# Kernel optimization log

Hardware: AMD Instinct MI355X
Metric: run time of the kernel (lower is better)

Reference implementation:

```python
import jax, jax.numpy as jnp
import numpy as np

D = 256      # d_size
Z = 32       # z_size
IN = 256     # input_size
B = 128      # minibatch_size
T = 1000     # seq_len
TAU = 2.0
W = 0.001    # w (KL weight, t>0)
W1 = 0.001   # w1 (KL weight, t==0)
WD1 = 0.001  # wd1 (init-h NLL weight)
EPS = 1e-6


def setup_inputs() -> dict:
    key = jax.random.key(0)
    ks = jax.random.split(key, 11)
    sD = 1.0 / np.sqrt(D)
    sZ = 1.0 / np.sqrt(Z)
    sI = 1.0 / np.sqrt(IN)
    return {
        "hd": jax.random.normal(ks[0], (B, T, IN), jnp.float32),
        "A": jax.random.normal(ks[1], (B, T, 2 * Z), jnp.float32) * 0.1,
        "in_p0": jax.random.normal(ks[2], (B, 2 * Z), jnp.float32) * 0.1,
        "noise": jax.random.normal(ks[3], (B, T, Z), jnp.float32),
        "Wd2h": jax.random.normal(ks[4], (D, D), jnp.float32) * sD,
        "Wz2h": jax.random.normal(ks[5], (D, Z), jnp.float32) * sZ,
        "Wd2z": jax.random.normal(ks[6], (2 * Z, D), jnp.float32) * sD,
        "Whd2h": jax.random.normal(ks[7], (D, IN), jnp.float32) * sI,
        "bias_d": jax.random.normal(ks[8], (D,), jnp.float32) * 0.1,
        "init_h": jax.random.normal(ks[9], (B, D), jnp.float32) * 0.1,
        "init_h_mu": jax.random.normal(ks[10], (D,), jnp.float32) * 0.1,
    }


def reference(hd, A, in_p0, noise, Wd2h, Wz2h, Wd2z, Whd2h, bias_d, init_h, init_h_mu):
    dtype = hd.dtype
    # tau vector: tau everywhere, 2*tau for first half of units
    tau = jnp.full((D,), TAU, dtype=dtype).at[: D // 2].set(2.0 * TAU)
    decay = 1.0 - 1.0 / tau
    inv_tau = 1.0 / tau

    # initialize(): wd1 != 0 -> h = init_h, d = tanh(h)
    h0 = init_h
    d0 = jnp.tanh(h0)

    def step(carry, xs):
        h, d = carry
        t, hd_t, A_t, n_t = xs
        # prior: t==0 uses external in_p, else d_to_z(d)
        dz = d @ Wd2z.T                              # [B, 2Z]
        prior_in = jnp.where(t == 0, in_p0, dz)
        mu_p = jnp.tanh(prior_in[:, :Z])
        sigma_p = jnp.exp(prior_in[:, Z:])
        # posterior from adaptive variables A
        mu_q = jnp.tanh(A_t[:, :Z])
        sigma_q = jnp.exp(A_t[:, Z:])
        # reparameterized sample
        z = mu_q + n_t * sigma_q
        # leaky-integrator MTRNN update
        pre = d @ Wd2h.T + z @ Wz2h.T + hd_t @ Whd2h.T + bias_d
        h_new = decay * h + pre * inv_tau
        d_new = jnp.tanh(h_new)
        # KL(q || p), normalized by z_size
        kl = jnp.sum(
            jnp.log(sigma_p + EPS) - jnp.log(sigma_q + EPS) - 0.5
            + 0.5 * (mu_q**2 + sigma_q**2 - 2.0 * mu_q * mu_p + mu_p**2)
            / (sigma_p**2 + EPS)
        ) / Z
        wkl = jnp.where(t == 0, W1, W) * kl
        return (h_new, d_new), (d_new, wkl)

    ts = jnp.arange(T)
    (_, _), (d_seq, wkls) = jax.lax.scan(
        step,
        (h0, d0),
        (ts, hd.transpose(1, 0, 2), A.transpose(1, 0, 2), noise.transpose(1, 0, 2)),
    )

    # compute_nll_init_h (init_var = 1.0)
    nll_init_h = jnp.sum(
        0.5 * jnp.log(2.0 * jnp.pi) + 0.5 * (init_h - init_h_mu) ** 2
    ) / D
    wnll_init_h = WD1 * nll_init_h

    return d_seq.transpose(1, 0, 2), jnp.sum(wkls), wnll_init_h
```

## Files before the change

kernel.cpp:

```cpp
#include <hip/hip_runtime.h>


#define BB 128
#define TT 1000
#define NSEQ 32768000
#define KEPS 1e-6f

typedef _Float16 half2v __attribute__((ext_vector_type(2)));

__device__ __forceinline__ float bfu(unsigned short u) {
    union { unsigned int i; float f; } v; v.i = ((unsigned int)u) << 16; return v.f;
}
__device__ __forceinline__ unsigned short f2bf(float f) {
    union { float f; unsigned int i; } v; v.f = f;
    unsigned int x = v.i;
    return (unsigned short)((x + 0x7fffu + ((x >> 16) & 1u)) >> 16);
}
__device__ __forceinline__ float ldf(const void* p, size_t i, int bf) {
    return bf ? bfu(((const unsigned short*)p)[i]) : ((const float*)p)[i];
}
__device__ __forceinline__ void stf(void* p, size_t i, float v, int bf) {
    if (bf) ((unsigned short*)p)[i] = f2bf(v);
    else    ((float*)p)[i] = v;
}
__device__ __forceinline__ half2v u2h2(unsigned int u) {
    union { unsigned int u; half2v h; } v; v.u = u; return v.h;
}
__device__ __forceinline__ half2v bfpair2h2(unsigned int u) {
    union { unsigned int i; float f; } lo, hi;
    lo.i = u << 16; hi.i = u & 0xffff0000u;
    half2v r; r.x = (_Float16)lo.f; r.y = (_Float16)hi.f; return r;
}
__device__ __forceinline__ unsigned short f2h_bits(float f) {
    union { _Float16 h; unsigned short u; } v; v.h = (_Float16)f; return v.u;
}

#if __has_builtin(__builtin_amdgcn_fdot2)
#define FDOT2(a, b, c) __builtin_amdgcn_fdot2((a), (b), (c), false)
#else
__device__ __forceinline__ float FDOT2(half2v a, half2v b, float c) {
    return c + (float)a.x * (float)b.x + (float)a.y * (float)b.y;
}
#endif

#define BAR() do {                                             \
    asm volatile("s_waitcnt lgkmcnt(0)" ::: "memory");         \
    __builtin_amdgcn_s_barrier();                              \
    asm volatile("" ::: "memory");                             \
} while (0)

__global__ __launch_bounds__(256) void k0_detect(
    const unsigned short* __restrict__ hd, int* __restrict__ flag)
{
    __shared__ int cnt;
    if (threadIdx.x == 0) cnt = 0;
    __syncthreads();
    int c = 0;
    for (int i = threadIdx.x; i < 2048; i += 256) {
        unsigned short u = hd[i];
        int e = (u >> 7) & 0xFF;
        c += ((e >= 112 && e <= 134) || ((u & 0x7FFF) == 0)) ? 1 : 0;
    }
    atomicAdd(&cnt, c);
    __syncthreads();
    if (threadIdx.x == 0) flag[0] = (cnt > 1700) ? 1 : 0;
}

__global__ __launch_bounds__(256) void k1_gemm(
    const void* __restrict__ hd,
    const void* __restrict__ W,
    const void* __restrict__ bias,
    void* __restrict__ out,
    const int* __restrict__ flagp)
{
    const int bf = flagp[0];
    __shared__ __align__(16) float hdS[32][36];
    const int tid = threadIdx.x;
    const int j = tid;
    const long m0 = (long)blockIdx.x * 32;
    const int lm = tid >> 3;
    const int lk = (tid & 7) * 4;

    float acc[32];
#pragma unroll
    for (int m = 0; m < 32; m++) acc[m] = 0.f;

    for (int kc = 0; kc < 256; kc += 32) {
        float stage[4];
        float w[32];
        if (bf) {
            const unsigned short* hp =
                (const unsigned short*)hd + (size_t)(m0 + lm) * 256 + kc + lk;
            uint2 sv = *(const uint2*)hp;
            stage[0] = bfu((unsigned short)(sv.x & 0xffff));
            stage[1] = bfu((unsigned short)(sv.x >> 16));
            stage[2] = bfu((unsigned short)(sv.y & 0xffff));
            stage[3] = bfu((unsigned short)(sv.y >> 16));
            const unsigned short* wp =
                (const unsigned short*)W + (size_t)j * 256 + kc;
#pragma unroll
            for (int g = 0; g < 4; g++) {
                uint4 wv = *(const uint4*)(wp + g * 8);
                w[g*8+0] = bfu((unsigned short)(wv.x & 0xffff));
                w[g*8+1] = bfu((unsigned short)(wv.x >> 16));
                w[g*8+2] = bfu((unsigned short)(wv.y & 0xffff));
                w[g*8+3] = bfu((unsigned short)(wv.y >> 16));
                w[g*8+4] = bfu((unsigned short)(wv.z & 0xffff));
                w[g*8+5] = bfu((unsigned short)(wv.z >> 16));
                w[g*8+6] = bfu((unsigned short)(wv.w & 0xffff));
                w[g*8+7] = bfu((unsigned short)(wv.w >> 16));
            }
        } else {
            const float* hp = (const float*)hd + (size_t)(m0 + lm) * 256 + kc + lk;
            float4 sv = *(const float4*)hp;
            stage[0] = sv.x; stage[1] = sv.y; stage[2] = sv.z; stage[3] = sv.w;
            const float* wp = (const float*)W + (size_t)j * 256 + kc;
#pragma unroll
            for (int g = 0; g < 8; g++) {
                float4 wv = *(const float4*)(wp + g * 4);
                w[g*4+0] = wv.x; w[g*4+1] = wv.y; w[g*4+2] = wv.z; w[g*4+3] = wv.w;
            }
        }
        __syncthreads();
#pragma unroll
        for (int q = 0; q < 4; q++) hdS[lm][lk + q] = stage[q];
        __syncthreads();
#pragma unroll
        for (int m = 0; m < 32; m++) {
            float s0 = 0.f, s1 = 0.f;
#pragma unroll
            for (int k4 = 0; k4 < 8; k4++) {
                float4 a = *(const float4*)&hdS[m][k4 * 4];
                float t0 = a.x*w[k4*4+0] + a.y*w[k4*4+1];
                float t1 = a.z*w[k4*4+2] + a.w*w[k4*4+3];
                if (k4 & 1) s1 += t0 + t1; else s0 += t0 + t1;
            }
            acc[m] += s0 + s1;
        }
    }
    float bj = ldf(bias, (size_t)j, bf);
#pragma unroll
    for (int m = 0; m < 32; m++)
        stf(out, (size_t)(m0 + m) * 256 + j, acc[m] + bj, bf);
}

__global__ __launch_bounds__(256) void k2_scan_bf(
    const unsigned short* __restrict__ A,
    const unsigned short* __restrict__ noise,
    const unsigned short* __restrict__ Wd2h,
    const unsigned short* __restrict__ Wz2h,
    const unsigned short* __restrict__ init_h,
    unsigned short* __restrict__ out,
    const int* __restrict__ flagp)
{
    if (flagp[0] != 1) return;
    const int b = blockIdx.x;
    const int tid = threadIdx.x;
    const int j = tid;
    const int l = tid & 63;
    const int w = tid >> 6;

    __shared__ unsigned int dPk[2][128];
    __shared__ unsigned int zPk[2][16];

    half2v wdh[128];
    {
        const uint4* wr = (const uint4*)(Wd2h + (size_t)j * 256);
#pragma unroll
        for (int k = 0; k < 32; k++) {
            uint4 q = wr[k];
            wdh[k*4+0] = bfpair2h2(q.x);
            wdh[k*4+1] = bfpair2h2(q.y);
            wdh[k*4+2] = bfpair2h2(q.z);
            wdh[k*4+3] = bfpair2h2(q.w);
        }
    }
    half2v wzh[16];
    {
        const uint4* wr = (const uint4*)(Wz2h + (size_t)j * 32);
#pragma unroll
        for (int k = 0; k < 4; k++) {
            uint4 q = wr[k];
            wzh[k*4+0] = bfpair2h2(q.x);
            wzh[k*4+1] = bfpair2h2(q.y);
            wzh[k*4+2] = bfpair2h2(q.z);
            wzh[k*4+3] = bfpair2h2(q.w);
        }
    }

    float hv = bfu(init_h[(size_t)b * 256 + j]);
    float h = hv;
    const float tau = (j < 128) ? 4.f : 2.f;
    const float decay = 1.f - 1.f / tau;
    const float invt = 1.f / tau;
    {
        float d0 = tanhf(hv);
        unsigned short u16 = f2h_bits(d0);
        int p16 = __shfl_xor((int)u16, 1, 64);
        if (!(tid & 1))
            dPk[0][tid >> 1] =
                (unsigned int)u16 | (((unsigned int)(unsigned short)p16) << 16);
    }

    const size_t baseA = (size_t)b * TT * 64;
    const size_t baseN = (size_t)b * TT * 32;
    const size_t baseO = (size_t)b * TT * 256;

    float aVc = 0.f, nVc = 0.f;
    if (w == 1) {
        float av0 = bfu(A[baseA + l]);
        float val0 = (l < 32) ? tanhf(av0) : expf(av0);
        float nv0 = (l < 32) ? bfu(noise[baseN + l]) : 0.f;
        float e0 = __shfl_down(val0, 32, 64);
        if (l < 32) {
            float z0 = val0 + nv0 * e0;
            unsigned short uz = f2h_bits(z0);
            int pz = __shfl_xor((int)uz, 1, 64);
            if (!(l & 1))
                zPk[0][l >> 1] =
                    (unsigned int)uz | (((unsigned int)(unsigned short)pz) << 16);
        }
        aVc = bfu(A[baseA + 64 + l]);
        nVc = (l < 32) ? bfu(noise[baseN + 32 + l]) : 0.f;
    }

    float hdw_c = bfu(out[baseO + j]);
    BAR();

#pragma unroll 1
    for (int t = 0; t < TT; t++) {
        float hdw_p = 0.f;
        if (t < TT - 1) hdw_p = bfu(out[baseO + (size_t)(t + 1) * 256 + j]);
        float aVp = 0.f, nVp = 0.f;
        if (w == 1 && t + 2 < TT) {
            aVp = bfu(A[baseA + (size_t)(t + 2) * 64 + l]);
            nVp = (l < 32) ? bfu(noise[baseN + (size_t)(t + 2) * 32 + l]) : 0.f;
        }

        float ac[8];
#pragma unroll
        for (int i = 0; i < 8; i++) ac[i] = 0.f;
        {
            const uint4* dp = (const uint4*)dPk[t & 1];
#pragma unroll
            for (int k = 0; k < 32; k++) {
                uint4 q = dp[k];
                const int base = (k & 1) << 2;
                ac[base+0] = FDOT2(u2h2(q.x), wdh[k*4+0], ac[base+0]);
                ac[base+1] = FDOT2(u2h2(q.y), wdh[k*4+1], ac[base+1]);
                ac[base+2] = FDOT2(u2h2(q.z), wdh[k*4+2], ac[base+2]);
                ac[base+3] = FDOT2(u2h2(q.w), wdh[k*4+3], ac[base+3]);
            }
            const uint4* zp = (const uint4*)zPk[t & 1];
#pragma unroll
            for (int k = 0; k < 4; k++) {
                uint4 q = zp[k];
                const int base = (k & 1) << 2;
                ac[base+0] = FDOT2(u2h2(q.x), wzh[k*4+0], ac[base+0]);
                ac[base+1] = FDOT2(u2h2(q.y), wzh[k*4+1], ac[base+1]);
                ac[base+2] = FDOT2(u2h2(q.z), wzh[k*4+2], ac[base+2]);
                ac[base+3] = FDOT2(u2h2(q.w), wzh[k*4+3], ac[base+3]);
            }
        }
        float P = ((ac[0] + ac[1]) + (ac[2] + ac[3]))
                + ((ac[4] + ac[5]) + (ac[6] + ac[7]));

        float pre = P + hdw_c;
        h = decay * h + pre * invt;
        float dn = tanhf(h);
        out[baseO + (size_t)t * 256 + j] = f2bf(dn);
        {
            unsigned short u16 = f2h_bits(dn);
            int p16 = __shfl_xor((int)u16, 1, 64);
            if (!(tid & 1))
                dPk[(t + 1) & 1][tid >> 1] =
                    (unsigned int)u16 | (((unsigned int)(unsigned short)p16) << 16);
        }
        if (w == 1 && t < TT - 1) {
            float val = (l < 32) ? tanhf(aVc) : expf(aVc);
            float e = __shfl_down(val, 32, 64);
            if (l < 32) {
                float zz = val + nVc * e;
                unsigned short uz = f2h_bits(zz);
                int pz = __shfl_xor((int)uz, 1, 64);
                if (!(l & 1))
                    zPk[(t + 1) & 1][l >> 1] =
                        (unsigned int)uz | (((unsigned int)(unsigned short)pz) << 16);
            }
            aVc = aVp; nVc = nVp;
        }
        hdw_c = hdw_p;
        BAR();
    }
}

__global__ __launch_bounds__(512) void k2_scan_f32(
    const float* __restrict__ A,
    const float* __restrict__ noise,
    const float* __restrict__ Wd2h,
    const float* __restrict__ Wz2h,
    const float* __restrict__ init_h,
    float* __restrict__ out,
    const int* __restrict__ flagp)
{
    if (flagp[0] != 0) return;
    const int b = blockIdx.x;
    const int tid = threadIdx.x;
    const int j = tid & 255;
    const int half = tid >> 8;
    const int isz = (tid >= 256 && tid < 288);
    const int zi = tid & 31;

    __shared__ __align__(16) float dS[256];
    __shared__ __align__(16) float zS[2][32];
    __shared__ float pp[2][256];

    float wdh[128];
#pragma unroll
    for (int u = 0; u < 128; u++)
        wdh[u] = Wd2h[(size_t)j * 256 + half * 128 + u];
    float wzh[16];
#pragma unroll
    for (int u = 0; u < 16; u++)
        wzh[u] = Wz2h[(size_t)j * 32 + half * 16 + u];

    const size_t baseA = (size_t)b * TT * 64;
    const size_t baseN = (size_t)b * TT * 32;
    const size_t baseO = (size_t)b * TT * 256;

    float h = 0.f, decay = 0.f, invt = 0.f;
    if (half == 0) {
        float hv = init_h[(size_t)b * 256 + j];
        h = hv;
        float tau = (j < 128) ? 4.f : 2.f;
        decay = 1.f - 1.f / tau;
        invt = 1.f / tau;
        dS[j] = tanhf(hv);
    }

    float aL = 0.f, aH = 0.f, nZ = 0.f;
    if (isz) {
        float a0 = A[baseA + zi];
        float a1 = A[baseA + 32 + zi];
        float n0 = noise[baseN + zi];
        zS[0][zi] = tanhf(a0) + n0 * expf(a1);
        aL = A[baseA + 64 + zi];
        aH = A[baseA + 64 + 32 + zi];
        nZ = noise[baseN + 32 + zi];
    }

    float hdw_c = 0.f;
    if (half == 0) hdw_c = out[baseO + j];
    BAR();

#pragma unroll 1
    for (int t = 0; t < TT; t++) {
        float hdw_p = 0.f;
        if (t < TT - 1 && half == 0)
            hdw_p = out[baseO + (size_t)(t + 1) * 256 + j];
        float aL2 = 0.f, aH2 = 0.f, nZ2 = 0.f;
        if (isz && t + 2 <= TT - 1) {
            aL2 = A[baseA + (size_t)(t + 2) * 64 + zi];
            aH2 = A[baseA + (size_t)(t + 2) * 64 + 32 + zi];
            nZ2 = noise[baseN + (size_t)(t + 2) * 32 + zi];
        }

        float pa0 = 0.f, pa1 = 0.f, pa2 = 0.f, pa3 = 0.f;
        const float* db = dS + half * 128;
#pragma unroll
        for (int g = 0; g < 16; g++) {
            float4 x = *(const float4*)(db + g * 8);
            float4 y = *(const float4*)(db + g * 8 + 4);
            float t0 = x.x*wdh[g*8+0] + x.y*wdh[g*8+1];
            float t1 = x.z*wdh[g*8+2] + x.w*wdh[g*8+3];
            float t2 = y.x*wdh[g*8+4] + y.y*wdh[g*8+5];
            float t3 = y.z*wdh[g*8+6] + y.w*wdh[g*8+7];
            float gs = (t0 + t1) + (t2 + t3);
            if      ((g & 3) == 0) pa0 += gs;
            else if ((g & 3) == 1) pa1 += gs;
            else if ((g & 3) == 2) pa2 += gs;
            else                   pa3 += gs;
        }
        {
            const float* zb = &zS[t & 1][half * 16];
            float4 z0 = *(const float4*)(zb);
            float4 z1 = *(const float4*)(zb + 4);
            float4 z2 = *(const float4*)(zb + 8);
            float4 z3 = *(const float4*)(zb + 12);
            float c0 = z0.x*wzh[0]  + z0.y*wzh[1];
            float c1 = z0.z*wzh[2]  + z0.w*wzh[3];
            float c2 = z1.x*wzh[4]  + z1.y*wzh[5];
            float c3 = z1.z*wzh[6]  + z1.w*wzh[7];
            float c4 = z2.x*wzh[8]  + z2.y*wzh[9];
            float c5 = z2.z*wzh[10] + z2.w*wzh[11];
            float c6 = z3.x*wzh[12] + z3.y*wzh[13];
            float c7 = z3.z*wzh[14] + z3.w*wzh[15];
            pa0 += (c0 + c1) + (c2 + c3);
            pa1 += (c4 + c5) + (c6 + c7);
        }
        pp[half][j] = (pa0 + pa1) + (pa2 + pa3);
        BAR();

        if (half == 0) {
            float pre = pp[0][j] + pp[1][j] + hdw_c;
            h = decay * h + pre * invt;
            float dn = tanhf(h);
            dS[j] = dn;
            out[baseO + (size_t)t * 256 + j] = dn;
        }
        if (isz && t < TT - 1) {
            zS[(t + 1) & 1][zi] = tanhf(aL) + nZ * expf(aH);
            aL = aL2; aH = aH2; nZ = nZ2;
        }
        hdw_c = hdw_p;
        BAR();
    }
}

__global__ __launch_bounds__(256) void k2b_kl(
    const void* __restrict__ dseq,
    const void* __restrict__ A,
    const void* __restrict__ in_p0,
    const void* __restrict__ Wd2z,
    float* __restrict__ ws_kl,
    const int* __restrict__ flagp)
{
    const int bf = flagp[0];
    const int tid = threadIdx.x;
    const long m0 = (long)blockIdx.x * 32;

    __shared__ __align__(16) float hdS[32][36];
    __shared__ float dzS[32][64];
    __shared__ float red[256];

    const int j  = tid & 63;
    const int rg = tid >> 6;

    const int lm = tid >> 3;
    const int lk = (tid & 7) * 4;
    const long gr_lm = m0 + lm;
    const int  t_lm  = (int)(gr_lm % 1000);
    const long prow  = (t_lm == 0) ? gr_lm : gr_lm - 1;

    float acc[8];
#pragma unroll
    for (int m = 0; m < 8; m++) acc[m] = 0.f;

    for (int kc = 0; kc < 256; kc += 32) {
        float stage[4];
        float w[32];
        if (bf) {
            const unsigned short* hp =
                (const unsigned short*)dseq + (size_t)prow * 256 + kc + lk;
            uint2 sv = *(const uint2*)hp;
            stage[0] = bfu((unsigned short)(sv.x & 0xffff));
            stage[1] = bfu((unsigned short)(sv.x >> 16));
            stage[2] = bfu((unsigned short)(sv.y & 0xffff));
            stage[3] = bfu((unsigned short)(sv.y >> 16));
            const unsigned short* wp =
                (const unsigned short*)Wd2z + (size_t)j * 256 + kc;
#pragma unroll
            for (int g = 0; g < 4; g++) {
                uint4 wv = *(const uint4*)(wp + g * 8);
                w[g*8+0] = bfu((unsigned short)(wv.x & 0xffff));
                w[g*8+1] = bfu((unsigned short)(wv.x >> 16));
                w[g*8+2] = bfu((unsigned short)(wv.y & 0xffff));
                w[g*8+3] = bfu((unsigned short)(wv.y >> 16));
                w[g*8+4] = bfu((unsigned short)(wv.z & 0xffff));
                w[g*8+5] = bfu((unsigned short)(wv.z >> 16));
                w[g*8+6] = bfu((unsigned short)(wv.w & 0xffff));
                w[g*8+7] = bfu((unsigned short)(wv.w >> 16));
            }
        } else {
            const float* hp = (const float*)dseq + (size_t)prow * 256 + kc + lk;
            float4 sv = *(const float4*)hp;
            stage[0] = sv.x; stage[1] = sv.y; stage[2] = sv.z; stage[3] = sv.w;
            const float* wp = (const float*)Wd2z + (size_t)j * 256 + kc;
#pragma unroll
            for (int g = 0; g < 8; g++) {
                float4 wv = *(const float4*)(wp + g * 4);
                w[g*4+0] = wv.x; w[g*4+1] = wv.y; w[g*4+2] = wv.z; w[g*4+3] = wv.w;
            }
        }
        __syncthreads();
#pragma unroll
        for (int q = 0; q < 4; q++) hdS[lm][lk + q] = stage[q];
        __syncthreads();
#pragma unroll
        for (int m = 0; m < 8; m++) {
            const int row = rg * 8 + m;
            float s0 = 0.f, s1 = 0.f;
#pragma unroll
            for (int k4 = 0; k4 < 8; k4++) {
                float4 a = *(const float4*)&hdS[row][k4 * 4];
                float t0 = a.x*w[k4*4+0] + a.y*w[k4*4+1];
                float t1 = a.z*w[k4*4+2] + a.w*w[k4*4+3];
                if (k4 & 1) s1 += t0 + t1; else s0 += t0 + t1;
            }
            acc[m] += s0 + s1;
        }
    }
    __syncthreads();
#pragma unroll
    for (int m = 0; m < 8; m++) dzS[rg * 8 + m][j] = acc[m];
    __syncthreads();

    const int zz = tid & 31;
    const int rr = tid >> 5;
    float s = 0.f;
#pragma unroll
    for (int mm = 0; mm < 4; mm++) {
        const int m = rr * 4 + mm;
        const long gr = m0 + m;
        const int  t  = (int)(gr % 1000);
        const long bb = gr / 1000;
        float pin_mu, pin_sg;
        if (t == 0) {
            pin_mu = ldf(in_p0, (size_t)bb * 64 + zz, bf);
            pin_sg = ldf(in_p0, (size_t)bb * 64 + 32 + zz, bf);
        } else {
            pin_mu = dzS[m][zz];
            pin_sg = dzS[m][zz + 32];
        }
        float mp = tanhf(pin_mu);
        float sp = expf(pin_sg);
        float amu = ldf(A, (size_t)gr * 64 + zz, bf);
        float asg = ldf(A, (size_t)gr * 64 + 32 + zz, bf);
        float mq = tanhf(amu);
        float sq = expf(asg);
        s += logf(sp + KEPS) - logf(sq + KEPS) - 0.5f
           + 0.5f * (mq*mq + sq*sq - 2.f*mq*mp + mp*mp) / (sp*sp + KEPS);
    }
    red[tid] = s;
    __syncthreads();
    for (int off = 128; off > 0; off >>= 1) {
        if (tid < off) red[tid] += red[tid + off];
        __syncthreads();
    }
    if (tid == 0) atomicAdd(ws_kl, red[0]);
}

__global__ __launch_bounds__(256) void k3_final(
    const void* __restrict__ init_h,
    const void* __restrict__ init_mu,
    const float* __restrict__ ws_kl,
    void* __restrict__ out,
    const int* __restrict__ flagp)
{
    const int bf = flagp[0];
    __shared__ float red[256];
    const int tid = threadIdx.x;
    float s = 0.f;
    for (int i = tid; i < BB * 256; i += 256) {
        float d = ldf(init_h, (size_t)i, bf) - ldf(init_mu, (size_t)(i & 255), bf);
        s += 0.5f * d * d;
    }
    red[tid] = s;
    __syncthreads();
    for (int off = 128; off > 0; off >>= 1) {
        if (tid < off) red[tid] += red[tid + off];
        __syncthreads();
    }
    if (tid == 0) {
        float tot = red[0] + (float)(BB * 256) * 0.91893853320467274f;
        stf(out, (size_t)NSEQ,     ws_kl[0] * (0.001f / 32.f), bf);
        stf(out, (size_t)NSEQ + 1, 0.001f * tot / 256.f, bf);
    }
}

extern "C" void kernel_launch(void* const* d_in, const int* in_sizes, int n_in,
                              void* d_out, int out_size, void* d_ws, size_t ws_size,
                              hipStream_t stream)
{
    float* wskl = (float*)d_ws;
    int*   flag = ((int*)d_ws) + 1;

    hipMemsetAsync(d_ws, 0, 8, stream);

    k0_detect<<<1, 256, 0, stream>>>((const unsigned short*)d_in[0], flag);

    k1_gemm<<<(BB * TT) / 32, 256, 0, stream>>>(d_in[0], d_in[7], d_in[8],
                                                d_out, flag);

    k2_scan_bf<<<BB, 256, 0, stream>>>(
        (const unsigned short*)d_in[1], (const unsigned short*)d_in[3],
        (const unsigned short*)d_in[4], (const unsigned short*)d_in[5],
        (const unsigned short*)d_in[9], (unsigned short*)d_out, flag);
    k2_scan_f32<<<BB, 512, 0, stream>>>(
        (const float*)d_in[1], (const float*)d_in[3],
        (const float*)d_in[4], (const float*)d_in[5],
        (const float*)d_in[9], (float*)d_out, flag);

    k2b_kl<<<(BB * TT) / 32, 256, 0, stream>>>(d_out, d_in[1], d_in[2],
                                               d_in[6], wskl, flag);

    k3_final<<<1, 256, 0, stream>>>(d_in[9], d_in[10], wskl, d_out, flag);
}
```

Measured before the change: 2.268 ms.

## Rewrite fp32 scan as single-pass 256-thread block with fast exp/tanh

```diff
diff --git a/kernel.cpp b/kernel.cpp
--- a/kernel.cpp
+++ b/kernel.cpp
@@ -42,6 +42,21 @@
     return c + (float)a.x * (float)b.x + (float)a.y * (float)b.y;
 }
 #endif
+
+__device__ __forceinline__ float fexp(float x) {
+    float e;
+    float t = x * 1.4426950408889634f;
+    asm("v_exp_f32 %0, %1" : "=v"(e) : "v"(t));
+    return e;
+}
+__device__ __forceinline__ float ftanh(float x) {
+    float e, r;
+    float t = x * 2.8853900817779268f;
+    asm("v_exp_f32 %0, %1" : "=v"(e) : "v"(t));
+    float d = e + 1.f;
+    asm("v_rcp_f32 %0, %1" : "=v"(r) : "v"(d));
+    return 1.f - 2.f * r;
+}
 
 #define BAR() do {                                             \
     asm volatile("s_waitcnt lgkmcnt(0)" ::: "memory");         \
@@ -142,6 +157,120 @@
 #pragma unroll
     for (int m = 0; m < 32; m++)
         stf(out, (size_t)(m0 + m) * 256 + j, acc[m] + bj, bf);
+}
+
+__global__ __launch_bounds__(256, 1) void k2_scan_f32(
+    const float* __restrict__ A,
+    const float* __restrict__ noise,
+    const float* __restrict__ Wd2h,
+    const float* __restrict__ Wz2h,
+    const float* __restrict__ init_h,
+    float* __restrict__ out,
+    const int* __restrict__ flagp)
+{
+    if (flagp[0] != 0) return;
+    const int b = blockIdx.x;
+    const int tid = threadIdx.x;
+    const int j = tid;
+    const int l = tid & 63;
+    const int w = tid >> 6;
+
+    __shared__ __align__(16) float dS[2][256];
+    __shared__ __align__(16) float zS[2][32];
+
+    float4 wdh[64];
+    {
+        const float4* wr = (const float4*)(Wd2h + (size_t)j * 256);
+#pragma unroll
+        for (int k = 0; k < 64; k++) wdh[k] = wr[k];
+    }
+    float4 wzh[8];
+    {
+        const float4* wr = (const float4*)(Wz2h + (size_t)j * 32);
+#pragma unroll
+        for (int k = 0; k < 8; k++) wzh[k] = wr[k];
+    }
+
+    const size_t baseA = (size_t)b * TT * 64;
+    const size_t baseN = (size_t)b * TT * 32;
+    const size_t baseO = (size_t)b * TT * 256;
+
+    float hv = init_h[(size_t)b * 256 + j];
+    float h = hv;
+    const float tau = (j < 128) ? 4.f : 2.f;
+    const float decay = 1.f - 1.f / tau;
+    const float invt = 1.f / tau;
+    dS[0][j] = ftanh(hv);
+
+    float aVc = 0.f, nVc = 0.f;
+    if (w == 1) {
+        float av0 = A[baseA + l];
+        float val0 = (l < 32) ? ftanh(av0) : fexp(av0);
+        float nv0 = (l < 32) ? noise[baseN + l] : 0.f;
+        float e0 = __shfl_down(val0, 32, 64);
+        if (l < 32) zS[0][l] = val0 + nv0 * e0;
+        aVc = A[baseA + 64 + l];
+        nVc = (l < 32) ? noise[baseN + 32 + l] : 0.f;
+    }
+
+    float hdw_c = out[baseO + j];
+    BAR();
+
+#pragma unroll 1
+    for (int t = 0; t < TT; t++) {
+        float hdw_p = 0.f;
+        if (t < TT - 1) hdw_p = out[baseO + (size_t)(t + 1) * 256 + j];
+        float aVp = 0.f, nVp = 0.f;
+        if (w == 1 && t + 2 < TT) {
+            aVp = A[baseA + (size_t)(t + 2) * 64 + l];
+            nVp = (l < 32) ? noise[baseN + (size_t)(t + 2) * 32 + l] : 0.f;
+        }
+
+        float ac[8];
+#pragma unroll
+        for (int i = 0; i < 8; i++) ac[i] = 0.f;
+        {
+            const float4* dp = (const float4*)dS[t & 1];
+#pragma unroll
+            for (int k = 0; k < 64; k++) {
+                float4 dv = dp[k];
+                float4 wv = wdh[k];
+                const int a = (k & 1) << 2;
+                ac[a+0] = fmaf(dv.x, wv.x, ac[a+0]);
+                ac[a+1] = fmaf(dv.y, wv.y, ac[a+1]);
+                ac[a+2] = fmaf(dv.z, wv.z, ac[a+2]);
+                ac[a+3] = fmaf(dv.w, wv.w, ac[a+3]);
+            }
+            const float4* zp = (const float4*)zS[t & 1];
+#pragma unroll
+            for (int k = 0; k < 8; k++) {
+                float4 zv = zp[k];
+                float4 wv = wzh[k];
+                const int a = (k & 1) << 2;
+                ac[a+0] = fmaf(zv.x, wv.x, ac[a+0]);
+                ac[a+1] = fmaf(zv.y, wv.y, ac[a+1]);
+                ac[a+2] = fmaf(zv.z, wv.z, ac[a+2]);
+                ac[a+3] = fmaf(zv.w, wv.w, ac[a+3]);
+            }
+        }
+        float P = ((ac[0] + ac[1]) + (ac[2] + ac[3]))
+                + ((ac[4] + ac[5]) + (ac[6] + ac[7]));
+
+        float pre = P + hdw_c;
+        h = decay * h + pre * invt;
+        float dn = ftanh(h);
+        out[baseO + (size_t)t * 256 + j] = dn;
+        dS[(t + 1) & 1][j] = dn;
+
+        if (w == 1 && t < TT - 1) {
+            float val = (l < 32) ? ftanh(aVc) : fexp(aVc);
+            float e = __shfl_down(val, 32, 64);
+            if (l < 32) zS[(t + 1) & 1][l] = val + nVc * e;
+            aVc = aVp; nVc = nVp;
+        }
+        hdw_c = hdw_p;
+        BAR();
+    }
 }
 
 __global__ __launch_bounds__(256) void k2_scan_bf(
@@ -194,7 +323,7 @@
     const float decay = 1.f - 1.f / tau;
     const float invt = 1.f / tau;
     {
-        float d0 = tanhf(hv);
+        float d0 = ftanh(hv);
         unsigned short u16 = f2h_bits(d0);
         int p16 = __shfl_xor((int)u16, 1, 64);
         if (!(tid & 1))
@@ -209,7 +338,7 @@
     float aVc = 0.f, nVc = 0.f;
     if (w == 1) {
         float av0 = bfu(A[baseA + l]);
-        float val0 = (l < 32) ? tanhf(av0) : expf(av0);
+        float val0 = (l < 32) ? ftanh(av0) : fexp(av0);
         float nv0 = (l < 32) ? bfu(noise[baseN + l]) : 0.f;
         float e0 = __shfl_down(val0, 32, 64);
         if (l < 32) {
@@ -267,7 +396,7 @@
 
         float pre = P + hdw_c;
         h = decay * h + pre * invt;
-        float dn = tanhf(h);
+        float dn = ftanh(h);
         out[baseO + (size_t)t * 256 + j] = f2bf(dn);
         {
             unsigned short u16 = f2h_bits(dn);
@@ -277,7 +406,7 @@
                     (unsigned int)u16 | (((unsigned int)(unsigned short)p16) << 16);
         }
         if (w == 1 && t < TT - 1) {
-            float val = (l < 32) ? tanhf(aVc) : expf(aVc);
+            float val = (l < 32) ? ftanh(aVc) : fexp(aVc);
             float e = __shfl_down(val, 32, 64);
             if (l < 32) {
                 float zz = val + nVc * e;
@@ -288,129 +417,6 @@
                         (unsigned int)uz | (((unsigned int)(unsigned short)pz) << 16);
             }
             aVc = aVp; nVc = nVp;
-        }
-        hdw_c = hdw_p;
-        BAR();
-    }
-}
-
-__global__ __launch_bounds__(512) void k2_scan_f32(
-    const float* __restrict__ A,
-    const float* __restrict__ noise,
-    const float* __restrict__ Wd2h,
-    const float* __restrict__ Wz2h,
-    const float* __restrict__ init_h,
-    float* __restrict__ out,
-    const int* __restrict__ flagp)
-{
-    if (flagp[0] != 0) return;
-    const int b = blockIdx.x;
-    const int tid = threadIdx.x;
-    const int j = tid & 255;
-    const int half = tid >> 8;
-    const int isz = (tid >= 256 && tid < 288);
-    const int zi = tid & 31;
-
-    __shared__ __align__(16) float dS[256];
-    __shared__ __align__(16) float zS[2][32];
-    __shared__ float pp[2][256];
-
-    float wdh[128];
-#pragma unroll
-    for (int u = 0; u < 128; u++)
-        wdh[u] = Wd2h[(size_t)j * 256 + half * 128 + u];
-    float wzh[16];
-#pragma unroll
-    for (int u = 0; u < 16; u++)
-        wzh[u] = Wz2h[(size_t)j * 32 + half * 16 + u];
-
-    const size_t baseA = (size_t)b * TT * 64;
-    const size_t baseN = (size_t)b * TT * 32;
-    const size_t baseO = (size_t)b * TT * 256;
-
-    float h = 0.f, decay = 0.f, invt = 0.f;
-    if (half == 0) {
-        float hv = init_h[(size_t)b * 256 + j];
-        h = hv;
-        float tau = (j < 128) ? 4.f : 2.f;
-        decay = 1.f - 1.f / tau;
-        invt = 1.f / tau;
-        dS[j] = tanhf(hv);
-    }
-
-    float aL = 0.f, aH = 0.f, nZ = 0.f;
-    if (isz) {
-        float a0 = A[baseA + zi];
-        float a1 = A[baseA + 32 + zi];
-        float n0 = noise[baseN + zi];
-        zS[0][zi] = tanhf(a0) + n0 * expf(a1);
-        aL = A[baseA + 64 + zi];
-        aH = A[baseA + 64 + 32 + zi];
-        nZ = noise[baseN + 32 + zi];
-    }
-
-    float hdw_c = 0.f;
-    if (half == 0) hdw_c = out[baseO + j];
-    BAR();
-
-#pragma unroll 1
-    for (int t = 0; t < TT; t++) {
-        float hdw_p = 0.f;
-        if (t < TT - 1 && half == 0)
-            hdw_p = out[baseO + (size_t)(t + 1) * 256 + j];
-        float aL2 = 0.f, aH2 = 0.f, nZ2 = 0.f;
-        if (isz && t + 2 <= TT - 1) {
-            aL2 = A[baseA + (size_t)(t + 2) * 64 + zi];
-            aH2 = A[baseA + (size_t)(t + 2) * 64 + 32 + zi];
-            nZ2 = noise[baseN + (size_t)(t + 2) * 32 + zi];
-        }
-
-        float pa0 = 0.f, pa1 = 0.f, pa2 = 0.f, pa3 = 0.f;
-        const float* db = dS + half * 128;
-#pragma unroll
-        for (int g = 0; g < 16; g++) {
-            float4 x = *(const float4*)(db + g * 8);
-            float4 y = *(const float4*)(db + g * 8 + 4);
-            float t0 = x.x*wdh[g*8+0] + x.y*wdh[g*8+1];
-            float t1 = x.z*wdh[g*8+2] + x.w*wdh[g*8+3];
-            float t2 = y.x*wdh[g*8+4] + y.y*wdh[g*8+5];
-            float t3 = y.z*wdh[g*8+6] + y.w*wdh[g*8+7];
-            float gs = (t0 + t1) + (t2 + t3);
-            if      ((g & 3) == 0) pa0 += gs;
-            else if ((g & 3) == 1) pa1 += gs;
-            else if ((g & 3) == 2) pa2 += gs;
-            else                   pa3 += gs;
-        }
-        {
-            const float* zb = &zS[t & 1][half * 16];
-            float4 z0 = *(const float4*)(zb);
-            float4 z1 = *(const float4*)(zb + 4);
-            float4 z2 = *(const float4*)(zb + 8);
-            float4 z3 = *(const float4*)(zb + 12);
-            float c0 = z0.x*wzh[0]  + z0.y*wzh[1];
-            float c1 = z0.z*wzh[2]  + z0.w*wzh[3];
-            float c2 = z1.x*wzh[4]  + z1.y*wzh[5];
-            float c3 = z1.z*wzh[6]  + z1.w*wzh[7];
-            float c4 = z2.x*wzh[8]  + z2.y*wzh[9];
-            float c5 = z2.z*wzh[10] + z2.w*wzh[11];
-            float c6 = z3.x*wzh[12] + z3.y*wzh[13];
-            float c7 = z3.z*wzh[14] + z3.w*wzh[15];
-            pa0 += (c0 + c1) + (c2 + c3);
-            pa1 += (c4 + c5) + (c6 + c7);
-        }
-        pp[half][j] = (pa0 + pa1) + (pa2 + pa3);
-        BAR();
-
-        if (half == 0) {
-            float pre = pp[0][j] + pp[1][j] + hdw_c;
-            h = decay * h + pre * invt;
-            float dn = tanhf(h);
-            dS[j] = dn;
-            out[baseO + (size_t)t * 256 + j] = dn;
-        }
-        if (isz && t < TT - 1) {
-            zS[(t + 1) & 1][zi] = tanhf(aL) + nZ * expf(aH);
-            aL = aL2; aH = aH2; nZ = nZ2;
         }
         hdw_c = hdw_p;
         BAR();
@@ -582,14 +588,14 @@
     k1_gemm<<<(BB * TT) / 32, 256, 0, stream>>>(d_in[0], d_in[7], d_in[8],
                                                 d_out, flag);
 
+    k2_scan_f32<<<BB, 256, 0, stream>>>(
+        (const float*)d_in[1], (const float*)d_in[3],
+        (const float*)d_in[4], (const float*)d_in[5],
+        (const float*)d_in[9], (float*)d_out, flag);
     k2_scan_bf<<<BB, 256, 0, stream>>>(
         (const unsigned short*)d_in[1], (const unsigned short*)d_in[3],
         (const unsigned short*)d_in[4], (const unsigned short*)d_in[5],
         (const unsigned short*)d_in[9], (unsigned short*)d_out, flag);
-    k2_scan_f32<<<BB, 512, 0, stream>>>(
-        (const float*)d_in[1], (const float*)d_in[3],
-        (const float*)d_in[4], (const float*)d_in[5],
-        (const float*)d_in[9], (float*)d_out, flag);
 
     k2b_kl<<<(BB * TT) / 32, 256, 0, stream>>>(d_out, d_in[1], d_in[2],
                                                d_in[6], wskl, flag);
```

New measurement: 3.590 ms. 58.3% more time.
